# Performance work log

Measured on AMD Instinct MI355X. Metric: run time of the kernel, lower is better.

Reference implementation:

```python
import jax, jax.numpy as jnp
import numpy as np

N, M, FEAT, GROUP, EMB = 512, 4096, 1024, 16, 64
DIM_GROUP = FEAT // GROUP  # 64


def _make_boxes(key, n):
    k1, k2, k3, k4 = jax.random.split(key, 4)
    cx = jax.random.uniform(k1, (n,), minval=0.0, maxval=800.0)
    cy = jax.random.uniform(k2, (n,), minval=0.0, maxval=800.0)
    w = jax.random.uniform(k3, (n,), minval=16.0, maxval=256.0)
    h = jax.random.uniform(k4, (n,), minval=16.0, maxval=256.0)
    return jnp.stack([cx - 0.5 * w, cy - 0.5 * h, cx + 0.5 * w, cy + 0.5 * h], axis=1)


def setup_inputs() -> dict:
    key = jax.random.key(0)
    ks = jax.random.split(key, 10)
    return {
        "roi_feat": jax.random.normal(ks[0], (N, FEAT), dtype=jnp.float32),
        "ref_feat": jax.random.normal(ks[1], (M, FEAT), dtype=jnp.float32),
        "rois_cur": _make_boxes(ks[2], N),
        "rois_ref": _make_boxes(ks[3], M),
        "Wg_w": jax.random.normal(ks[4], (GROUP, EMB), dtype=jnp.float32) * 0.01,
        "Wg_b": jnp.zeros((GROUP,), dtype=jnp.float32),
        "Wq_w": jax.random.normal(ks[5], (FEAT, FEAT), dtype=jnp.float32) * (1.0 / np.sqrt(FEAT)),
        "Wq_b": jnp.zeros((FEAT,), dtype=jnp.float32),
        "Wk_w": jax.random.normal(ks[6], (FEAT, FEAT), dtype=jnp.float32) * (1.0 / np.sqrt(FEAT)),
        "Wk_b": jnp.zeros((FEAT,), dtype=jnp.float32),
        "Wv_w": jax.random.normal(ks[7], (FEAT, FEAT), dtype=jnp.float32) * 0.01,  # grouped 1x1 conv: [16 groups x 64 out, 1024 in-per-group]
        "Wv_b": jnp.zeros((FEAT,), dtype=jnp.float32),
    }


def _position_embedding(bbox, ref_bbox):
    # extract_position_matrix
    xmin, ymin, xmax, ymax = [ref_bbox[:, i] for i in range(4)]
    w_ref = xmax - xmin + 1.0
    h_ref = ymax - ymin + 1.0
    cx_ref = 0.5 * (xmin + xmax)
    cy_ref = 0.5 * (ymin + ymax)
    xmin, ymin, xmax, ymax = [bbox[:, i] for i in range(4)]
    w = xmax - xmin + 1.0
    h = ymax - ymin + 1.0
    cx = 0.5 * (xmin + xmax)
    cy = 0.5 * (ymin + ymax)
    dx = jnp.log(jnp.abs((cx[:, None] - cx_ref[None, :]) / w[:, None]) + 0.001)
    dy = jnp.log(jnp.abs((cy[:, None] - cy_ref[None, :]) / h[:, None]) + 0.001)
    dw = jnp.log(w[:, None] / w_ref[None, :])
    dh = jnp.log(h[:, None] / h_ref[None, :])
    pos = jnp.stack([dx, dy, dw, dh], axis=2)  # [N, M, 4]
    # extract_position_embedding with feat_dim=64, wave_length=1000
    feat_range = jnp.arange(EMB // 8, dtype=jnp.float32)  # 8
    dim_mat = jnp.power(1000.0, (8.0 / EMB) * feat_range)  # [8]
    div = (pos * 100.0)[..., None] / dim_mat  # [N, M, 4, 8]
    emb = jnp.concatenate([jnp.sin(div), jnp.cos(div)], axis=3)  # [N, M, 4, 16]
    return emb.reshape(pos.shape[0], pos.shape[1], EMB)  # [N, M, 64]


def reference(roi_feat, ref_feat, rois_cur, rois_ref,
              Wg_w, Wg_b, Wq_w, Wq_b, Wk_w, Wk_b, Wv_w, Wv_b):
    emb = _position_embedding(rois_cur, rois_ref)  # [N, M, 64]
    # Wg: 1x1 conv over embedding channels -> per-group bias [N, G, M]
    aff_weight = jax.nn.relu(jnp.einsum('nme,ge->ngm', emb, Wg_w) + Wg_b[None, :, None])
    q = (roi_feat @ Wq_w.T + Wq_b).reshape(-1, GROUP, DIM_GROUP)  # [N, G, dg]
    k = (ref_feat @ Wk_w.T + Wk_b).reshape(-1, GROUP, DIM_GROUP)  # [M, G, dg]
    aff_scale = jnp.einsum('ngd,mgd->ngm', q, k) * (1.0 / np.sqrt(DIM_GROUP))
    weighted_aff = jnp.log(aff_weight + 1e-6) + aff_scale
    aff_softmax = jax.nn.softmax(weighted_aff, axis=2)  # [N, G, M]
    out_t = jnp.einsum('ngm,mf->ngf', aff_softmax, ref_feat)  # [N, G, FEAT]
    # grouped 1x1 conv Wv: group g maps its FEAT inputs to DIM_GROUP outputs
    Wv_g = Wv_w.reshape(GROUP, DIM_GROUP, FEAT)
    output = jnp.einsum('ngf,gof->ngo', out_t, Wv_g).reshape(-1, FEAT) + Wv_b
    return output
```

## Files before the change

### kernel.cpp

```cpp
#include <hip/hip_runtime.h>
#include <hip/hip_bf16.h>

#define N_ROI 512
#define M_REF 4096
#define FEAT 1024
#define GROUP 16
#define DG 64
#define EMB 64
#define BP 68
#define GLDH 72

using f16x8 = __attribute__((ext_vector_type(8))) _Float16;
using f16x4 = __attribute__((ext_vector_type(4))) _Float16;
using f32x4 = __attribute__((ext_vector_type(4))) float;

__global__ __launch_bounds__(256) void cast_f16_5(
    const float* __restrict__ s0, _Float16* __restrict__ d0, int n0,
    const float* __restrict__ s1, _Float16* __restrict__ d1, int n1,
    const float* __restrict__ s2, _Float16* __restrict__ d2, int n2,
    const float* __restrict__ s3, _Float16* __restrict__ d3, int n3,
    const float* __restrict__ s4, _Float16* __restrict__ d4, int n4) {
  const int q0 = n0 >> 2, q1 = n1 >> 2, q2 = n2 >> 2, q3 = n3 >> 2, q4 = n4 >> 2;
  const int total = q0 + q1 + q2 + q3 + q4;
  for (int i = blockIdx.x * 256 + threadIdx.x; i < total;
       i += gridDim.x * 256) {
    int j = i;
    const float* s;
    _Float16* d;
    if (j < q0) { s = s0; d = d0; }
    else { j -= q0;
      if (j < q1) { s = s1; d = d1; }
      else { j -= q1;
        if (j < q2) { s = s2; d = d2; }
        else { j -= q2;
          if (j < q3) { s = s3; d = d3; }
          else { j -= q3; s = s4; d = d4; } } } }
    float4 v = *(const float4*)&s[(size_t)j * 4];
    *(f16x4*)&d[(size_t)j * 4] =
        f16x4{(_Float16)v.x, (_Float16)v.y, (_Float16)v.z, (_Float16)v.w};
  }
}

__global__ __launch_bounds__(256) void gemm_ff16(
    const _Float16* __restrict__ A, const _Float16* __restrict__ B,
    const float* __restrict__ bias, _Float16* __restrict__ C,
    int M, int N, int K) {
  __shared__ _Float16 As[128 * GLDH];
  __shared__ _Float16 Bs[64 * GLDH];
  const int tid = threadIdx.x, lane = tid & 63, wid = tid >> 6;
  const int bm = blockIdx.y * 128, bn = blockIdx.x * 64;
  const int wr = (wid >> 1) * 64, wc = (wid & 1) * 32;
  const int lrow = lane & 15, lk = (lane >> 4) * 8;

  f16x8 ra[4], rb[2];
#pragma unroll
  for (int i = 0; i < 4; ++i) {
    int idx = tid + i * 256, r = idx >> 3, c = (idx & 7) * 8;
    ra[i] = *(const f16x8*)&A[(size_t)(bm + r) * K + c];
  }
#pragma unroll
  for (int i = 0; i < 2; ++i) {
    int idx = tid + i * 256, r = idx >> 3, c = (idx & 7) * 8;
    rb[i] = *(const f16x8*)&B[(size_t)(bn + r) * K + c];
  }

  f32x4 acc[4][2] = {};
  for (int k0 = 0; k0 < K; k0 += 64) {
#pragma unroll
    for (int i = 0; i < 4; ++i) {
      int idx = tid + i * 256, r = idx >> 3, c = (idx & 7) * 8;
      *(f16x8*)&As[r * GLDH + c] = ra[i];
    }
#pragma unroll
    for (int i = 0; i < 2; ++i) {
      int idx = tid + i * 256, r = idx >> 3, c = (idx & 7) * 8;
      *(f16x8*)&Bs[r * GLDH + c] = rb[i];
    }
    __syncthreads();
    if (k0 + 64 < K) {
#pragma unroll
      for (int i = 0; i < 4; ++i) {
        int idx = tid + i * 256, r = idx >> 3, c = (idx & 7) * 8;
        ra[i] = *(const f16x8*)&A[(size_t)(bm + r) * K + k0 + 64 + c];
      }
#pragma unroll
      for (int i = 0; i < 2; ++i) {
        int idx = tid + i * 256, r = idx >> 3, c = (idx & 7) * 8;
        rb[i] = *(const f16x8*)&B[(size_t)(bn + r) * K + k0 + 64 + c];
      }
    }
    f16x8 a[4][2], b[2][2];
#pragma unroll
    for (int mi = 0; mi < 4; ++mi)
#pragma unroll
      for (int ks = 0; ks < 2; ++ks)
        a[mi][ks] = *(const f16x8*)&As[(wr + mi * 16 + lrow) * GLDH + ks * 32 + lk];
#pragma unroll
    for (int ni = 0; ni < 2; ++ni)
#pragma unroll
      for (int ks = 0; ks < 2; ++ks)
        b[ni][ks] = *(const f16x8*)&Bs[(wc + ni * 16 + lrow) * GLDH + ks * 32 + lk];
#pragma unroll
    for (int ks = 0; ks < 2; ++ks)
#pragma unroll
      for (int mi = 0; mi < 4; ++mi)
#pragma unroll
        for (int ni = 0; ni < 2; ++ni)
          acc[mi][ni] = __builtin_amdgcn_mfma_f32_16x16x32_f16(
              a[mi][ks], b[ni][ks], acc[mi][ni], 0, 0, 0);
    __syncthreads();
  }
#pragma unroll
  for (int mi = 0; mi < 4; ++mi)
#pragma unroll
    for (int ni = 0; ni < 2; ++ni) {
      int col = bn + wc + ni * 16 + lrow;
      float bv = bias ? bias[col] : 0.0f;
#pragma unroll
      for (int i = 0; i < 4; ++i) {
        int row = bm + wr + mi * 16 + (lane >> 4) * 4 + i;
        C[(size_t)row * N + col] = (_Float16)(acc[mi][ni][i] + bv);
      }
    }
}

__global__ __launch_bounds__(256) void s_fused_kernel(
    const float* __restrict__ rois_cur, const float* __restrict__ rois_ref,
    const float* __restrict__ Wg_w, const float* __restrict__ Wg_b,
    const _Float16* __restrict__ q, const _Float16* __restrict__ k,
    float* __restrict__ S) {
  __shared__ _Float16 Bias[GROUP][16][BP];
  const int tid = threadIdx.x;
  const int lane = tid & 63, w = tid >> 6;
  const int n0 = blockIdx.x * 16, m0 = blockIdx.y * 64;
  const int lm = lane & 15, lc = lane >> 4;
  const int wm = w * 16;
  const int mglob = m0 + wm + lm;

  f16x8 wgf[2];
#pragma unroll
  for (int kc = 0; kc < 2; ++kc) {
    const float* p = Wg_w + lm * EMB + kc * 32 + lc * 8;
#pragma unroll
    for (int j = 0; j < 8; ++j) wgf[kc][j] = (_Float16)p[j];
  }
  float wgb[4];
#pragma unroll
  for (int i = 0; i < 4; ++i) wgb[i] = Wg_b[lc * 4 + i];

  const float4 rb = reinterpret_cast<const float4*>(rois_ref)[mglob];
  const float wr_ = rb.z - rb.x + 1.0f, hr_ = rb.w - rb.y + 1.0f;
  const float cxr = 0.5f * (rb.x + rb.z), cyr = 0.5f * (rb.y + rb.w);
  const float lwr = __logf(wr_), lhr = __logf(hr_);

  const float inv_dim[8] = {1.0f,          0.42169651f,  0.17782794f,
                            0.074989417f,  0.031622776f, 0.013335214f,
                            0.0056234133f, 0.0023713737f};
  const int isY = lc >> 1;
  const int useCos = lc & 1;

#pragma unroll 2
  for (int nl = 0; nl < 16; ++nl) {
    const int n = n0 + nl;
    const float x0 = rois_cur[n * 4 + 0], y0 = rois_cur[n * 4 + 1];
    const float x1 = rois_cur[n * 4 + 2], y1 = rois_cur[n * 4 + 3];
    const float ww = x1 - x0 + 1.0f, hh = y1 - y0 + 1.0f;
    const float cx = 0.5f * (x0 + x1), cy = 0.5f * (y0 + y1);
    float pa, pb;
    if (isY) {
      pa = __logf(fabsf((cy - cyr) / hh) + 0.001f);
      pb = __logf(hh) - lhr;
    } else {
      pa = __logf(fabsf((cx - cxr) / ww) + 0.001f);
      pb = __logf(ww) - lwr;
    }
    pa *= 100.0f;
    pb *= 100.0f;
    f16x8 ef0, ef1;
#pragma unroll
    for (int f = 0; f < 8; ++f) {
      const float xa = pa * inv_dim[f];
      const float xb = pb * inv_dim[f];
      ef0[f] = (_Float16)(useCos ? __cosf(xa) : __sinf(xa));
      ef1[f] = (_Float16)(useCos ? __cosf(xb) : __sinf(xb));
    }
    f32x4 acc = {};
    acc = __builtin_amdgcn_mfma_f32_16x16x32_f16(wgf[0], ef0, acc, 0, 0, 0);
    acc = __builtin_amdgcn_mfma_f32_16x16x32_f16(wgf[1], ef1, acc, 0, 0, 0);
#pragma unroll
    for (int i = 0; i < 4; ++i) {
      float v = fmaxf(acc[i] + wgb[i], 0.0f);
      Bias[lc * 4 + i][nl][wm + lm] = (_Float16)__logf(v + 1e-6f);
    }
  }

#pragma unroll 2
  for (int g = 0; g < GROUP; ++g) {
    f16x8 qa0 = *(const f16x8*)&q[(size_t)(n0 + lm) * FEAT + g * DG + lc * 8];
    f16x8 qa1 = *(const f16x8*)&q[(size_t)(n0 + lm) * FEAT + g * DG + 32 + lc * 8];
    f16x8 kb0 = *(const f16x8*)&k[(size_t)mglob * FEAT + g * DG + lc * 8];
    f16x8 kb1 = *(const f16x8*)&k[(size_t)mglob * FEAT + g * DG + 32 + lc * 8];
    f32x4 acc = {};
    acc = __builtin_amdgcn_mfma_f32_16x16x32_f16(qa0, kb0, acc, 0, 0, 0);
    acc = __builtin_amdgcn_mfma_f32_16x16x32_f16(qa1, kb1, acc, 0, 0, 0);
#pragma unroll
    for (int i = 0; i < 4; ++i) {
      const int r = lc * 4 + i;
      float bl = (float)Bias[g][r][wm + lm];
      S[((size_t)(n0 + r) * GROUP + g) * M_REF + m0 + wm + lm] =
          bl + acc[i] * 0.125f;
    }
  }
}

__global__ __launch_bounds__(512) void pv_fused_kernel(
    const float* __restrict__ S, const _Float16* __restrict__ vt,
    const float* __restrict__ Wv_b, float* __restrict__ out) {
  __shared__ float wacc[8][16][64];
  __shared__ float wm_[8][16], wl_[8][16];
  const int tid = threadIdx.x, lane = tid & 63, w = tid >> 6;
  const int n0 = blockIdx.x * 16, g = blockIdx.y;
  const int lm = lane & 15, lc = lane >> 4;
  const size_t srow = ((size_t)(n0 + lm) * GROUP + g) * M_REF;

  f32x4 acc[4] = {};
  float mrun = -1e30f, lrun = 0.0f;

#pragma unroll 2
  for (int mc = 0; mc < 16; ++mc) {
    const int mb = w * 512 + mc * 32;
    const float4 sa = *(const float4*)&S[srow + mb + lc * 8];
    const float4 sb = *(const float4*)&S[srow + mb + lc * 8 + 4];
    float cmax = fmaxf(fmaxf(fmaxf(sa.x, sa.y), fmaxf(sa.z, sa.w)),
                       fmaxf(fmaxf(sb.x, sb.y), fmaxf(sb.z, sb.w)));
    cmax = fmaxf(cmax, __shfl_xor(cmax, 16));
    cmax = fmaxf(cmax, __shfl_xor(cmax, 32));
    const float mnew = fmaxf(mrun, cmax);
    const float fac = __expf(mrun - mnew);
    float p[8];
    p[0] = __expf(sa.x - mnew); p[1] = __expf(sa.y - mnew);
    p[2] = __expf(sa.z - mnew); p[3] = __expf(sa.w - mnew);
    p[4] = __expf(sb.x - mnew); p[5] = __expf(sb.y - mnew);
    p[6] = __expf(sb.z - mnew); p[7] = __expf(sb.w - mnew);
    float csum = ((p[0] + p[1]) + (p[2] + p[3])) + ((p[4] + p[5]) + (p[6] + p[7]));
    csum += __shfl_xor(csum, 16);
    csum += __shfl_xor(csum, 32);
    lrun = lrun * fac + csum;
    mrun = mnew;
    f16x8 af;
#pragma unroll
    for (int j = 0; j < 8; ++j) af[j] = (_Float16)p[j];
    float fr[4];
#pragma unroll
    for (int i = 0; i < 4; ++i) fr[i] = __shfl(fac, lc * 4 + i);
#pragma unroll
    for (int ct = 0; ct < 4; ++ct) {
      f16x8 bf = *(const f16x8*)
          &vt[(size_t)(g * DG + ct * 16 + lm) * M_REF + mb + lc * 8];
#pragma unroll
      for (int i = 0; i < 4; ++i) acc[ct][i] *= fr[i];
      acc[ct] = __builtin_amdgcn_mfma_f32_16x16x32_f16(af, bf, acc[ct], 0, 0, 0);
    }
  }

#pragma unroll
  for (int ct = 0; ct < 4; ++ct)
#pragma unroll
    for (int i = 0; i < 4; ++i)
      wacc[w][lc * 4 + i][ct * 16 + lm] = acc[ct][i];
  if (lane < 16) {
    wm_[w][lane] = mrun;
    wl_[w][lane] = lrun;
  }
  __syncthreads();

  if (tid < 256) {
    const int r = tid >> 4, c0 = (tid & 15) * 4;
    float M = -1e30f;
#pragma unroll
    for (int ww = 0; ww < 8; ++ww) M = fmaxf(M, wm_[ww][r]);
    float e[8], D = 0.0f;
#pragma unroll
    for (int ww = 0; ww < 8; ++ww) {
      e[ww] = __expf(wm_[ww][r] - M);
      D += e[ww] * wl_[ww][r];
    }
    const float inv = 1.0f / D;
    float4 o;
    float* po = &o.x;
#pragma unroll
    for (int j = 0; j < 4; ++j) {
      float s = 0.0f;
#pragma unroll
      for (int ww = 0; ww < 8; ++ww) s += e[ww] * wacc[ww][r][c0 + j];
      po[j] = s * inv + Wv_b[g * DG + c0 + j];
    }
    *(float4*)&out[(size_t)(n0 + r) * FEAT + g * DG + c0] = o;
  }
}

extern "C" void kernel_launch(void* const* d_in, const int* in_sizes, int n_in,
                              void* d_out, int out_size, void* d_ws,
                              size_t ws_size, hipStream_t stream) {
  const float* roi_feat = (const float*)d_in[0];
  const float* ref_feat = (const float*)d_in[1];
  const float* rois_cur = (const float*)d_in[2];
  const float* rois_ref = (const float*)d_in[3];
  const float* Wg_w = (const float*)d_in[4];
  const float* Wg_b = (const float*)d_in[5];
  const float* Wq_w = (const float*)d_in[6];
  const float* Wq_b = (const float*)d_in[7];
  const float* Wk_w = (const float*)d_in[8];
  const float* Wk_b = (const float*)d_in[9];
  const float* Wv_w = (const float*)d_in[10];
  const float* Wv_b = (const float*)d_in[11];
  float* out = (float*)d_out;

  _Float16* q16 = (_Float16*)d_ws;
  _Float16* k16 = q16 + (size_t)N_ROI * FEAT;
  _Float16* vt16 = k16 + (size_t)M_REF * FEAT;
  _Float16* roi16 = vt16 + (size_t)FEAT * M_REF;
  _Float16* ref16 = roi16 + (size_t)N_ROI * FEAT;
  _Float16* wq16 = ref16 + (size_t)M_REF * FEAT;
  _Float16* wk16 = wq16 + (size_t)FEAT * FEAT;
  _Float16* wv16 = wk16 + (size_t)FEAT * FEAT;
  float* S = (float*)(wv16 + (size_t)FEAT * FEAT);

  cast_f16_5<<<dim3(2048), 256, 0, stream>>>(
      roi_feat, roi16, N_ROI * FEAT, ref_feat, ref16, M_REF * FEAT,
      Wq_w, wq16, FEAT * FEAT, Wk_w, wk16, FEAT * FEAT,
      Wv_w, wv16, FEAT * FEAT);

  gemm_ff16<<<dim3(FEAT / 64, N_ROI / 128), 256, 0, stream>>>(
      roi16, wq16, Wq_b, q16, N_ROI, FEAT, FEAT);
  gemm_ff16<<<dim3(FEAT / 64, M_REF / 128), 256, 0, stream>>>(
      ref16, wk16, Wk_b, k16, M_REF, FEAT, FEAT);
  gemm_ff16<<<dim3(M_REF / 64, FEAT / 128), 256, 0, stream>>>(
      wv16, ref16, nullptr, vt16, FEAT, M_REF, FEAT);

  s_fused_kernel<<<dim3(N_ROI / 16, M_REF / 64), 256, 0, stream>>>(
      rois_cur, rois_ref, Wg_w, Wg_b, q16, k16, S);

  pv_fused_kernel<<<dim3(N_ROI / 16, GROUP), 512, 0, stream>>>(
      S, vt16, Wv_b, out);
}
```

Measured before the change: 272.7 us.

## Fuse score computation with online softmax and PV into split-M flash kernel

Merges the score kernel and the softmax·V kernel into one flash-attention-style kernel. Each block handles 16 queries, all groups, and one eighth of the reference range, and a small combine kernel merges the partial max, sum and accumulators. This removes writing and re-reading the large fp32 score tensor through global memory. In exchange the grid has few blocks, each with serial chunk loops and barriers, and adds a partial-result buffer and a second launch.

```diff
diff --git a/kernel.cpp b/kernel.cpp
--- a/kernel.cpp
+++ b/kernel.cpp
@@ -7,8 +7,12 @@
 #define GROUP 16
 #define DG 64
 #define EMB 64
-#define BP 68
 #define GLDH 72
+#define MSPLIT 8
+#define MRANGE (M_REF / MSPLIT)
+#define MCHUNK 128
+#define BP2 136
+#define PTP 40
 
 using f16x8 = __attribute__((ext_vector_type(8))) _Float16;
 using f16x4 = __attribute__((ext_vector_type(4))) _Float16;
@@ -124,18 +128,21 @@
     }
 }
 
-__global__ __launch_bounds__(256) void s_fused_kernel(
+__global__ __launch_bounds__(512) void attn_fused_kernel(
     const float* __restrict__ rois_cur, const float* __restrict__ rois_ref,
     const float* __restrict__ Wg_w, const float* __restrict__ Wg_b,
     const _Float16* __restrict__ q, const _Float16* __restrict__ k,
-    float* __restrict__ S) {
-  __shared__ _Float16 Bias[GROUP][16][BP];
-  const int tid = threadIdx.x;
-  const int lane = tid & 63, w = tid >> 6;
-  const int n0 = blockIdx.x * 16, m0 = blockIdx.y * 64;
+    const _Float16* __restrict__ vt, float* __restrict__ pacc,
+    float* __restrict__ pml) {
+  __shared__ _Float16 Bias[GROUP][16][BP2];
+  __shared__ _Float16 pt[8][16][PTP];
+  const int tid = threadIdx.x, lane = tid & 63, w = tid >> 6;
+  const int bid = blockIdx.x;
+  const int split = bid & 7, nt = bid >> 3;
+  const int n0 = nt * 16;
+  const int mb0 = split * MRANGE;
   const int lm = lane & 15, lc = lane >> 4;
-  const int wm = w * 16;
-  const int mglob = m0 + wm + lm;
+  const int g0 = w * 2;
 
   f16x8 wgf[2];
 #pragma unroll
@@ -148,10 +155,16 @@
 #pragma unroll
   for (int i = 0; i < 4; ++i) wgb[i] = Wg_b[lc * 4 + i];
 
-  const float4 rb = reinterpret_cast<const float4*>(rois_ref)[mglob];
-  const float wr_ = rb.z - rb.x + 1.0f, hr_ = rb.w - rb.y + 1.0f;
-  const float cxr = 0.5f * (rb.x + rb.z), cyr = 0.5f * (rb.y + rb.w);
-  const float lwr = __logf(wr_), lhr = __logf(hr_);
+  f16x8 qb[2][2];
+#pragma unroll
+  for (int gi = 0; gi < 2; ++gi)
+#pragma unroll
+    for (int kc = 0; kc < 2; ++kc)
+      qb[gi][kc] = *(const f16x8*)
+          &q[(size_t)(n0 + lm) * FEAT + (g0 + gi) * DG + kc * 32 + lc * 8];
+
+  f32x4 acc[2][4] = {};
+  float mrun[2] = {-1e30f, -1e30f}, lrun[2] = {0.0f, 0.0f};
 
   const float inv_dim[8] = {1.0f,          0.42169651f,  0.17782794f,
                             0.074989417f,  0.031622776f, 0.013335214f,
@@ -159,144 +172,167 @@
   const int isY = lc >> 1;
   const int useCos = lc & 1;
 
-#pragma unroll 2
-  for (int nl = 0; nl < 16; ++nl) {
-    const int n = n0 + nl;
-    const float x0 = rois_cur[n * 4 + 0], y0 = rois_cur[n * 4 + 1];
-    const float x1 = rois_cur[n * 4 + 2], y1 = rois_cur[n * 4 + 3];
-    const float ww = x1 - x0 + 1.0f, hh = y1 - y0 + 1.0f;
-    const float cx = 0.5f * (x0 + x1), cy = 0.5f * (y0 + y1);
-    float pa, pb;
-    if (isY) {
-      pa = __logf(fabsf((cy - cyr) / hh) + 0.001f);
-      pb = __logf(hh) - lhr;
-    } else {
-      pa = __logf(fabsf((cx - cxr) / ww) + 0.001f);
-      pb = __logf(ww) - lwr;
-    }
-    pa *= 100.0f;
-    pb *= 100.0f;
-    f16x8 ef0, ef1;
-#pragma unroll
-    for (int f = 0; f < 8; ++f) {
-      const float xa = pa * inv_dim[f];
-      const float xb = pb * inv_dim[f];
-      ef0[f] = (_Float16)(useCos ? __cosf(xa) : __sinf(xa));
-      ef1[f] = (_Float16)(useCos ? __cosf(xb) : __sinf(xb));
-    }
-    f32x4 acc = {};
-    acc = __builtin_amdgcn_mfma_f32_16x16x32_f16(wgf[0], ef0, acc, 0, 0, 0);
-    acc = __builtin_amdgcn_mfma_f32_16x16x32_f16(wgf[1], ef1, acc, 0, 0, 0);
-#pragma unroll
-    for (int i = 0; i < 4; ++i) {
-      float v = fmaxf(acc[i] + wgb[i], 0.0f);
-      Bias[lc * 4 + i][nl][wm + lm] = (_Float16)__logf(v + 1e-6f);
-    }
-  }
-
-#pragma unroll 2
-  for (int g = 0; g < GROUP; ++g) {
-    f16x8 qa0 = *(const f16x8*)&q[(size_t)(n0 + lm) * FEAT + g * DG + lc * 8];
-    f16x8 qa1 = *(const f16x8*)&q[(size_t)(n0 + lm) * FEAT + g * DG + 32 + lc * 8];
-    f16x8 kb0 = *(const f16x8*)&k[(size_t)mglob * FEAT + g * DG + lc * 8];
-    f16x8 kb1 = *(const f16x8*)&k[(size_t)mglob * FEAT + g * DG + 32 + lc * 8];
-    f32x4 acc = {};
-    acc = __builtin_amdgcn_mfma_f32_16x16x32_f16(qa0, kb0, acc, 0, 0, 0);
-    acc = __builtin_amdgcn_mfma_f32_16x16x32_f16(qa1, kb1, acc, 0, 0, 0);
-#pragma unroll
-    for (int i = 0; i < 4; ++i) {
-      const int r = lc * 4 + i;
-      float bl = (float)Bias[g][r][wm + lm];
-      S[((size_t)(n0 + r) * GROUP + g) * M_REF + m0 + wm + lm] =
-          bl + acc[i] * 0.125f;
-    }
-  }
-}
-
-__global__ __launch_bounds__(512) void pv_fused_kernel(
-    const float* __restrict__ S, const _Float16* __restrict__ vt,
+  for (int ch = 0; ch < MRANGE / MCHUNK; ++ch) {
+    const int cb = mb0 + ch * MCHUNK;
+    const int mglob = cb + w * 16 + lm;
+
+    const float4 rb = reinterpret_cast<const float4*>(rois_ref)[mglob];
+    const float wr_ = rb.z - rb.x + 1.0f, hr_ = rb.w - rb.y + 1.0f;
+    const float cxr = 0.5f * (rb.x + rb.z), cyr = 0.5f * (rb.y + rb.w);
+    const float lwr = __logf(wr_), lhr = __logf(hr_);
+
+    __syncthreads();
+
+    for (int nl = 0; nl < 16; ++nl) {
+      const int n = n0 + nl;
+      const float x0 = rois_cur[n * 4 + 0], y0 = rois_cur[n * 4 + 1];
+      const float x1 = rois_cur[n * 4 + 2], y1 = rois_cur[n * 4 + 3];
+      const float ww = x1 - x0 + 1.0f, hh = y1 - y0 + 1.0f;
+      const float cx = 0.5f * (x0 + x1), cy = 0.5f * (y0 + y1);
+      float pa, pb;
+      if (isY) {
+        pa = __logf(fabsf((cy - cyr) / hh) + 0.001f);
+        pb = __logf(hh) - lhr;
+      } else {
+        pa = __logf(fabsf((cx - cxr) / ww) + 0.001f);
+        pb = __logf(ww) - lwr;
+      }
+      pa *= 100.0f;
+      pb *= 100.0f;
+      f16x8 ef0, ef1;
+#pragma unroll
+      for (int f = 0; f < 8; ++f) {
+        const float xa = pa * inv_dim[f];
+        const float xb = pb * inv_dim[f];
+        ef0[f] = (_Float16)(useCos ? __cosf(xa) : __sinf(xa));
+        ef1[f] = (_Float16)(useCos ? __cosf(xb) : __sinf(xb));
+      }
+      f32x4 bacc = {};
+      bacc = __builtin_amdgcn_mfma_f32_16x16x32_f16(wgf[0], ef0, bacc, 0, 0, 0);
+      bacc = __builtin_amdgcn_mfma_f32_16x16x32_f16(wgf[1], ef1, bacc, 0, 0, 0);
+#pragma unroll
+      for (int i = 0; i < 4; ++i) {
+        float v = fmaxf(bacc[i] + wgb[i], 0.0f);
+        Bias[lc * 4 + i][nl][w * 16 + lm] = (_Float16)__logf(v + 1e-6f);
+      }
+    }
+    __syncthreads();
+
+    for (int st = 0; st < 4; ++st) {
+      const int ms = cb + st * 32;
+#pragma unroll
+      for (int gi = 0; gi < 2; ++gi) {
+        const int g = g0 + gi;
+        const size_t kbase = (size_t)(ms + lm) * FEAT + g * DG + lc * 8;
+        f16x8 ka0a = *(const f16x8*)&k[kbase];
+        f16x8 ka0b = *(const f16x8*)&k[kbase + 32];
+        f16x8 ka1a = *(const f16x8*)&k[kbase + (size_t)16 * FEAT];
+        f16x8 ka1b = *(const f16x8*)&k[kbase + (size_t)16 * FEAT + 32];
+        f32x4 sAa = {}, sBa = {};
+        sAa = __builtin_amdgcn_mfma_f32_16x16x32_f16(ka0a, qb[gi][0], sAa, 0, 0, 0);
+        sAa = __builtin_amdgcn_mfma_f32_16x16x32_f16(ka0b, qb[gi][1], sAa, 0, 0, 0);
+        sBa = __builtin_amdgcn_mfma_f32_16x16x32_f16(ka1a, qb[gi][0], sBa, 0, 0, 0);
+        sBa = __builtin_amdgcn_mfma_f32_16x16x32_f16(ka1b, qb[gi][1], sBa, 0, 0, 0);
+        const f16x4 bA = *(const f16x4*)&Bias[g][lm][st * 32 + lc * 4];
+        const f16x4 bB = *(const f16x4*)&Bias[g][lm][st * 32 + 16 + lc * 4];
+        float s[8];
+#pragma unroll
+        for (int i = 0; i < 4; ++i) {
+          s[i] = (float)bA[i] + sAa[i] * 0.125f;
+          s[4 + i] = (float)bB[i] + sBa[i] * 0.125f;
+        }
+        float cmax = s[0];
+#pragma unroll
+        for (int i = 1; i < 8; ++i) cmax = fmaxf(cmax, s[i]);
+        cmax = fmaxf(cmax, __shfl_xor(cmax, 16));
+        cmax = fmaxf(cmax, __shfl_xor(cmax, 32));
+        const float mnew = fmaxf(mrun[gi], cmax);
+        const float fac = __expf(mrun[gi] - mnew);
+        float p[8];
+        float csum = 0.0f;
+#pragma unroll
+        for (int i = 0; i < 8; ++i) {
+          p[i] = __expf(s[i] - mnew);
+          csum += p[i];
+        }
+        csum += __shfl_xor(csum, 16);
+        csum += __shfl_xor(csum, 32);
+        lrun[gi] = lrun[gi] * fac + csum;
+        mrun[gi] = mnew;
+        float fr[4];
+#pragma unroll
+        for (int i = 0; i < 4; ++i) fr[i] = __shfl(fac, lc * 4 + i);
+#pragma unroll
+        for (int ct = 0; ct < 4; ++ct)
+#pragma unroll
+          for (int i = 0; i < 4; ++i) acc[gi][ct][i] *= fr[i];
+        f16x4 pA = {(_Float16)p[0], (_Float16)p[1], (_Float16)p[2], (_Float16)p[3]};
+        f16x4 pB = {(_Float16)p[4], (_Float16)p[5], (_Float16)p[6], (_Float16)p[7]};
+        *(f16x4*)&pt[w][lm][lc * 4] = pA;
+        *(f16x4*)&pt[w][lm][16 + lc * 4] = pB;
+        const f16x8 pfrag = *(const f16x8*)&pt[w][lm][lc * 8];
+#pragma unroll
+        for (int ct = 0; ct < 4; ++ct) {
+          const f16x8 vf = *(const f16x8*)
+              &vt[(size_t)(g * DG + ct * 16 + lm) * M_REF + ms + lc * 8];
+          acc[gi][ct] = __builtin_amdgcn_mfma_f32_16x16x32_f16(pfrag, vf,
+                                                              acc[gi][ct], 0, 0, 0);
+        }
+      }
+    }
+  }
+
+#pragma unroll
+  for (int gi = 0; gi < 2; ++gi) {
+    const size_t base = (size_t)(nt * GROUP + g0 + gi) * MSPLIT + split;
+#pragma unroll
+    for (int ct = 0; ct < 4; ++ct)
+#pragma unroll
+      for (int i = 0; i < 4; ++i)
+        pacc[(base * 16 + lc * 4 + i) * 64 + ct * 16 + lm] = acc[gi][ct][i];
+    if (lc == 0) {
+      pml[(base * 16 + lm) * 2 + 0] = mrun[gi];
+      pml[(base * 16 + lm) * 2 + 1] = lrun[gi];
+    }
+  }
+}
+
+__global__ __launch_bounds__(256) void combine_kernel(
+    const float* __restrict__ pacc, const float* __restrict__ pml,
     const float* __restrict__ Wv_b, float* __restrict__ out) {
-  __shared__ float wacc[8][16][64];
-  __shared__ float wm_[8][16], wl_[8][16];
-  const int tid = threadIdx.x, lane = tid & 63, w = tid >> 6;
-  const int n0 = blockIdx.x * 16, g = blockIdx.y;
-  const int lm = lane & 15, lc = lane >> 4;
-  const size_t srow = ((size_t)(n0 + lm) * GROUP + g) * M_REF;
-
-  f32x4 acc[4] = {};
-  float mrun = -1e30f, lrun = 0.0f;
-
-#pragma unroll 2
-  for (int mc = 0; mc < 16; ++mc) {
-    const int mb = w * 512 + mc * 32;
-    const float4 sa = *(const float4*)&S[srow + mb + lc * 8];
-    const float4 sb = *(const float4*)&S[srow + mb + lc * 8 + 4];
-    float cmax = fmaxf(fmaxf(fmaxf(sa.x, sa.y), fmaxf(sa.z, sa.w)),
-                       fmaxf(fmaxf(sb.x, sb.y), fmaxf(sb.z, sb.w)));
-    cmax = fmaxf(cmax, __shfl_xor(cmax, 16));
-    cmax = fmaxf(cmax, __shfl_xor(cmax, 32));
-    const float mnew = fmaxf(mrun, cmax);
-    const float fac = __expf(mrun - mnew);
-    float p[8];
-    p[0] = __expf(sa.x - mnew); p[1] = __expf(sa.y - mnew);
-    p[2] = __expf(sa.z - mnew); p[3] = __expf(sa.w - mnew);
-    p[4] = __expf(sb.x - mnew); p[5] = __expf(sb.y - mnew);
-    p[6] = __expf(sb.z - mnew); p[7] = __expf(sb.w - mnew);
-    float csum = ((p[0] + p[1]) + (p[2] + p[3])) + ((p[4] + p[5]) + (p[6] + p[7]));
-    csum += __shfl_xor(csum, 16);
-    csum += __shfl_xor(csum, 32);
-    lrun = lrun * fac + csum;
-    mrun = mnew;
-    f16x8 af;
-#pragma unroll
-    for (int j = 0; j < 8; ++j) af[j] = (_Float16)p[j];
-    float fr[4];
-#pragma unroll
-    for (int i = 0; i < 4; ++i) fr[i] = __shfl(fac, lc * 4 + i);
-#pragma unroll
-    for (int ct = 0; ct < 4; ++ct) {
-      f16x8 bf = *(const f16x8*)
-          &vt[(size_t)(g * DG + ct * 16 + lm) * M_REF + mb + lc * 8];
-#pragma unroll
-      for (int i = 0; i < 4; ++i) acc[ct][i] *= fr[i];
-      acc[ct] = __builtin_amdgcn_mfma_f32_16x16x32_f16(af, bf, acc[ct], 0, 0, 0);
-    }
-  }
-
-#pragma unroll
-  for (int ct = 0; ct < 4; ++ct)
-#pragma unroll
-    for (int i = 0; i < 4; ++i)
-      wacc[w][lc * 4 + i][ct * 16 + lm] = acc[ct][i];
-  if (lane < 16) {
-    wm_[w][lane] = mrun;
-    wl_[w][lane] = lrun;
-  }
-  __syncthreads();
-
-  if (tid < 256) {
-    const int r = tid >> 4, c0 = (tid & 15) * 4;
-    float M = -1e30f;
-#pragma unroll
-    for (int ww = 0; ww < 8; ++ww) M = fmaxf(M, wm_[ww][r]);
-    float e[8], D = 0.0f;
-#pragma unroll
-    for (int ww = 0; ww < 8; ++ww) {
-      e[ww] = __expf(wm_[ww][r] - M);
-      D += e[ww] * wl_[ww][r];
-    }
-    const float inv = 1.0f / D;
-    float4 o;
-    float* po = &o.x;
-#pragma unroll
-    for (int j = 0; j < 4; ++j) {
-      float s = 0.0f;
-#pragma unroll
-      for (int ww = 0; ww < 8; ++ww) s += e[ww] * wacc[ww][r][c0 + j];
-      po[j] = s * inv + Wv_b[g * DG + c0 + j];
-    }
-    *(float4*)&out[(size_t)(n0 + r) * FEAT + g * DG + c0] = o;
-  }
+  const int nt = blockIdx.x >> 4, g = blockIdx.x & 15;
+  const int r = threadIdx.x >> 4, c0 = (threadIdx.x & 15) * 4;
+  const size_t gb = (size_t)(nt * GROUP + g) * MSPLIT;
+
+  float ms[MSPLIT], ls[MSPLIT];
+  float M = -1e30f;
+#pragma unroll
+  for (int s = 0; s < MSPLIT; ++s) {
+    ms[s] = pml[((gb + s) * 16 + r) * 2 + 0];
+    ls[s] = pml[((gb + s) * 16 + r) * 2 + 1];
+    M = fmaxf(M, ms[s]);
+  }
+  float e[MSPLIT], D = 0.0f;
+#pragma unroll
+  for (int s = 0; s < MSPLIT; ++s) {
+    e[s] = __expf(ms[s] - M);
+    D += e[s] * ls[s];
+  }
+  const float inv = 1.0f / D;
+  float4 o = {0.0f, 0.0f, 0.0f, 0.0f};
+  float* po = &o.x;
+#pragma unroll
+  for (int s = 0; s < MSPLIT; ++s) {
+    const float4 a = *(const float4*)&pacc[((gb + s) * 16 + r) * 64 + c0];
+    po[0] += e[s] * a.x;
+    po[1] += e[s] * a.y;
+    po[2] += e[s] * a.z;
+    po[3] += e[s] * a.w;
+  }
+#pragma unroll
+  for (int j = 0; j < 4; ++j)
+    po[j] = po[j] * inv + Wv_b[g * DG + c0 + j];
+  *(float4*)&out[(size_t)(nt * 16 + r) * FEAT + g * DG + c0] = o;
 }
 
 extern "C" void kernel_launch(void* const* d_in, const int* in_sizes, int n_in,
@@ -324,7 +360,8 @@
   _Float16* wq16 = ref16 + (size_t)M_REF * FEAT;
   _Float16* wk16 = wq16 + (size_t)FEAT * FEAT;
   _Float16* wv16 = wk16 + (size_t)FEAT * FEAT;
-  float* S = (float*)(wv16 + (size_t)FEAT * FEAT);
+  float* pacc = (float*)(wv16 + (size_t)FEAT * FEAT);
+  float* pml = pacc + (size_t)N_ROI * GROUP * MSPLIT * 64;
 
   cast_f16_5<<<dim3(2048), 256, 0, stream>>>(
       roi_feat, roi16, N_ROI * FEAT, ref_feat, ref16, M_REF * FEAT,
@@ -338,9 +375,9 @@
   gemm_ff16<<<dim3(M_REF / 64, FEAT / 128), 256, 0, stream>>>(
       wv16, ref16, nullptr, vt16, FEAT, M_REF, FEAT);
 
-  s_fused_kernel<<<dim3(N_ROI / 16, M_REF / 64), 256, 0, stream>>>(
-      rois_cur, rois_ref, Wg_w, Wg_b, q16, k16, S);
-
-  pv_fused_kernel<<<dim3(N_ROI / 16, GROUP), 512, 0, stream>>>(
-      S, vt16, Wv_b, out);
-}
+  attn_fused_kernel<<<dim3((N_ROI / 16) * MSPLIT), 512, 0, stream>>>(
+      rois_cur, rois_ref, Wg_w, Wg_b, q16, k16, vt16, pacc, pml);
+
+  combine_kernel<<<dim3((N_ROI / 16) * GROUP), 256, 0, stream>>>(
+      pacc, pml, Wv_b, out);
+}
```

New measurement: 275.9 us. Within noise of the previous version (+1.2%).
